# Kernel tuning notes

Hardware: AMD Instinct MI355X
Metric: run time of the kernel (lower is better)

The kernel has to match this reference:

```python
import jax, jax.numpy as jnp
import numpy as np

N = 100000
E = 1600000
D_IN = 128
D_H = 128


def _glorot(key, shape):
    fan_in, fan_out = shape[1], shape[0]
    lim = np.sqrt(6.0 / (fan_in + fan_out))
    return jax.random.uniform(key, shape, jnp.float32, -lim, lim)


def setup_inputs() -> dict:
    key = jax.random.key(0)
    ks = jax.random.split(key, 12)
    x = jax.random.normal(ks[0], (N, D_IN), jnp.float32)
    edge_index = jax.random.randint(ks[1], (2, E), 0, N, jnp.int64)
    return {
        "x": x,
        "edge_index": edge_index,
        # lin1, lin2 (nn.Linear: y = x @ W.T + b)
        "W1": _glorot(ks[2], (D_H, D_IN)),
        "b1": jnp.zeros((D_H,), jnp.float32),
        "W2": _glorot(ks[3], (D_H, D_H)),
        "b2": jnp.zeros((D_H,), jnp.float32),
        # SAGEConv1: lin_l (neighbors, with bias), lin_r (root, no bias)
        "c1_Wl": _glorot(ks[4], (D_H, D_H)),
        "c1_bl": jnp.zeros((D_H,), jnp.float32),
        "c1_Wr": _glorot(ks[5], (D_H, D_H)),
        # SAGEConv2
        "c2_Wl": _glorot(ks[6], (D_H, D_H)),
        "c2_bl": jnp.zeros((D_H,), jnp.float32),
        "c2_Wr": _glorot(ks[7], (D_H, D_H)),
    }


def _sage_conv(h, src, dst, Wl, bl, Wr, num_nodes):
    # PyG SAGEConv (mean aggr): out = lin_l(mean_{j in N(i)} h_j) + lin_r(h_i)
    msgs = h[src]  # [E, D] gather
    agg = jax.ops.segment_sum(msgs, dst, num_segments=num_nodes)  # [N, D]
    deg = jax.ops.segment_sum(jnp.ones((src.shape[0],), h.dtype), dst,
                              num_segments=num_nodes)
    mean = agg / jnp.maximum(deg, 1.0)[:, None]
    return mean @ Wl.T + bl + h @ Wr.T


def reference(x, edge_index, W1, b1, W2, b2,
              c1_Wl, c1_bl, c1_Wr, c2_Wl, c2_bl, c2_Wr):
    src, dst = edge_index[0], edge_index[1]
    n = x.shape[0]
    h = jax.nn.relu(x @ W1.T + b1)
    h = jax.nn.relu(_sage_conv(h, src, dst, c1_Wl, c1_bl, c1_Wr, n))
    h = jax.nn.relu(h @ W2.T + b2)
    h = jax.nn.relu(_sage_conv(h, src, dst, c2_Wl, c2_bl, c2_Wr, n))
    return h
```

## Files before the change

### kernel.cpp

```cpp
#include <hip/hip_runtime.h>
#include <hip/hip_bf16.h>

#define NN 100000
#define EE 1600000
#define DD 128

#define BSH 9
#define NBUK ((NN + 511) / 512)
#define EPB 8192

typedef __attribute__((ext_vector_type(8))) _Float16 half8;
typedef __attribute__((ext_vector_type(2))) _Float16 half2v;
typedef __attribute__((ext_vector_type(4))) float f32x4;

__global__ void k_detect(const long long* __restrict__ ei64, int* __restrict__ flag) {
    __shared__ int ok;
    if (threadIdx.x == 0) ok = 1;
    __syncthreads();
    long long v = ei64[threadIdx.x];
    if (v < 0 || v >= (long long)NN) atomicAnd(&ok, 0);
    __syncthreads();
    if (threadIdx.x == 0) *flag = ok;
}

__device__ inline int load_edge(const int* ei32, const long long* ei64, int is64, size_t pos) {
    return is64 ? (int)ei64[pos] : ei32[pos];
}

__global__ __launch_bounds__(1024) void k_bhist(const int* __restrict__ ei32,
                                                const long long* __restrict__ ei64,
                                                const int* __restrict__ flag,
                                                int* __restrict__ bcnt) {
    __shared__ int h[NBUK];
    int t = threadIdx.x;
    if (t < NBUK) h[t] = 0;
    __syncthreads();
    int is64 = *flag;
    int base = blockIdx.x * EPB;
    int end = min(base + EPB, EE);
    for (int e = base + t; e < end; e += 1024) {
        int d = load_edge(ei32, ei64, is64, (size_t)EE + e);
        atomicAdd(&h[d >> BSH], 1);
    }
    __syncthreads();
    if (t < NBUK && h[t] > 0) atomicAdd(&bcnt[t], h[t]);
}

__global__ __launch_bounds__(256) void k_bscan(const int* __restrict__ bcnt,
                                               int* __restrict__ bbase,
                                               int* __restrict__ bcur) {
    __shared__ int sm[256];
    int t = threadIdx.x;
    int v = (t < NBUK) ? bcnt[t] : 0;
    sm[t] = v;
    __syncthreads();
    for (int off = 1; off < 256; off <<= 1) {
        int u = (t >= off) ? sm[t - off] : 0;
        __syncthreads();
        sm[t] += u;
        __syncthreads();
    }
    if (t < NBUK) {
        int b = sm[t] - v;
        bbase[t] = b;
        bcur[t] = b;
    }
    if (t == 0) bbase[NBUK] = EE;
}

__global__ __launch_bounds__(1024) void k_part(const int* __restrict__ ei32,
                                               const long long* __restrict__ ei64,
                                               const int* __restrict__ flag,
                                               int* __restrict__ bcur,
                                               unsigned* __restrict__ eb) {
    __shared__ int h[NBUK];
    __shared__ int cbase[NBUK];
    int t = threadIdx.x;
    if (t < NBUK) h[t] = 0;
    __syncthreads();
    int is64 = *flag;
    int base = blockIdx.x * EPB;
    int end = min(base + EPB, EE);
    int mys[8], myd[8];
    int cnt_i = 0;
    for (int e = base + t; e < end; e += 1024) {
        int s = load_edge(ei32, ei64, is64, (size_t)e);
        int d = load_edge(ei32, ei64, is64, (size_t)EE + e);
        mys[cnt_i] = s;
        myd[cnt_i] = d;
        ++cnt_i;
        atomicAdd(&h[d >> BSH], 1);
    }
    __syncthreads();
    if (t < NBUK && h[t] > 0) cbase[t] = atomicAdd(&bcur[t], h[t]);
    __syncthreads();
    if (t < NBUK) h[t] = 0;
    __syncthreads();
    for (int i = 0; i < cnt_i; ++i) {
        int b = myd[i] >> BSH;
        int slot = atomicAdd(&h[b], 1);
        unsigned v = (unsigned)mys[i] | ((unsigned)(myd[i] & 511) << 17);
        eb[cbase[b] + slot] = v;
    }
}

__global__ __launch_bounds__(1024) void k_bucket(const unsigned* __restrict__ eb,
                                                 const int* __restrict__ bbase,
                                                 int* __restrict__ rp,
                                                 int* __restrict__ ssrc) {
    __shared__ int ncnt[512];
    __shared__ int cur[512];
    int b = blockIdx.x, t = threadIdx.x;
    int ebeg = bbase[b], eend = bbase[b + 1];
    int nodeBase = b << BSH;
    int nNodes = min(512, NN - nodeBase);
    if (t < 512) ncnt[t] = 0;
    __syncthreads();
    for (int i = ebeg + t; i < eend; i += 1024) {
        unsigned v = eb[i];
        atomicAdd(&ncnt[v >> 17], 1);
    }
    __syncthreads();
    int own = (t < 512) ? ncnt[t] : 0;
    for (int off = 1; off < 512; off <<= 1) {
        int u = (t >= off && t < 512) ? ncnt[t - off] : 0;
        __syncthreads();
        if (t < 512) ncnt[t] += u;
        __syncthreads();
    }
    if (t < 512) {
        int excl = ncnt[t] - own;
        cur[t] = ebeg + excl;
        if (t < nNodes) rp[nodeBase + t] = ebeg + excl;
    }
    __syncthreads();
    for (int i = ebeg + t; i < eend; i += 1024) {
        unsigned v = eb[i];
        int slot = atomicAdd(&cur[v >> 17], 1);
        ssrc[slot] = (int)(v & 0x1FFFFu);
    }
    if (b == 0 && t == 0) rp[NN] = EE;
}

__global__ void k_prepw(const float* __restrict__ w0, const float* __restrict__ w1,
                        const float* __restrict__ w2, const float* __restrict__ w3,
                        const float* __restrict__ w4, const float* __restrict__ w5,
                        _Float16* __restrict__ whi) {
    int i = blockIdx.x * 256 + threadIdx.x;
    if (i >= 6 * 16384) return;
    int slot = i >> 14, idx = i & 16383;
    const float* w = slot == 0 ? w0 : slot == 1 ? w1 : slot == 2 ? w2
                   : slot == 3 ? w3 : slot == 4 ? w4 : w5;
    whi[i] = (_Float16)w[idx];
}

#define WSTR 136

template <bool DUAL, bool AF16, bool OF16>
__global__ __launch_bounds__(256) void k_gemm(const void* __restrict__ A,
                                              const _Float16* __restrict__ W1g,
                                              const void* __restrict__ A2,
                                              const _Float16* __restrict__ W2g,
                                              const float* __restrict__ bias,
                                              void* __restrict__ out) {
    __shared__ _Float16 sW[128 * WSTR];
    int t = threadIdx.x;
    int wave = t >> 6;
    int lane = t & 63;
    int lr = lane & 15;
    int lk = lane >> 4;
    int rowBase = blockIdx.x * 128 + wave * 32;

    f32x4 acc[2][8];
#pragma unroll
    for (int mt = 0; mt < 2; ++mt)
#pragma unroll
        for (int nt = 0; nt < 8; ++nt) acc[mt][nt] = (f32x4){0.f, 0.f, 0.f, 0.f};

    const int NPASS = DUAL ? 2 : 1;
    for (int pass = 0; pass < NPASS; ++pass) {
        const _Float16* Wg = pass ? W2g : W1g;
        const void* Ap = pass ? A2 : A;
        if (pass) __syncthreads();
#pragma unroll
        for (int i = 0; i < 8; ++i) {
            int c = t + i * 256;
            int n = c >> 4, j = c & 15;
            *(half8*)(sW + n * WSTR + j * 8) = *(const half8*)(Wg + n * 128 + j * 8);
        }
        __syncthreads();

#pragma unroll
        for (int ks = 0; ks < 4; ++ks) {
            int kf = ks * 32 + lk * 8;
            half8 b[8];
#pragma unroll
            for (int nt = 0; nt < 8; ++nt)
                b[nt] = *(const half8*)(sW + (nt * 16 + lr) * WSTR + (ks * 4 + lk) * 8);
#pragma unroll
            for (int mt = 0; mt < 2; ++mt) {
                int row = rowBase + mt * 16 + lr;
                int rc = row < NN ? row : NN - 1;
                if (AF16) {
                    half8 a = *(const half8*)((const _Float16*)Ap + (size_t)rc * 128 + kf);
#pragma unroll
                    for (int nt = 0; nt < 8; ++nt)
                        acc[mt][nt] = __builtin_amdgcn_mfma_f32_16x16x32_f16(a, b[nt], acc[mt][nt], 0, 0, 0);
                } else {
                    const float* ap = (const float*)Ap + (size_t)rc * 128 + kf;
                    float4 a0 = *(const float4*)ap;
                    float4 a1 = *(const float4*)(ap + 4);
                    float av[8] = {a0.x, a0.y, a0.z, a0.w, a1.x, a1.y, a1.z, a1.w};
                    half8 ah, al;
#pragma unroll
                    for (int j = 0; j < 8; ++j) {
                        _Float16 h = (_Float16)av[j];
                        ah[j] = h;
                        al[j] = (_Float16)(av[j] - (float)h);
                    }
#pragma unroll
                    for (int nt = 0; nt < 8; ++nt) {
                        acc[mt][nt] = __builtin_amdgcn_mfma_f32_16x16x32_f16(ah, b[nt], acc[mt][nt], 0, 0, 0);
                        acc[mt][nt] = __builtin_amdgcn_mfma_f32_16x16x32_f16(al, b[nt], acc[mt][nt], 0, 0, 0);
                    }
                }
            }
        }
    }

#pragma unroll
    for (int mt = 0; mt < 2; ++mt) {
#pragma unroll
        for (int nt = 0; nt < 8; ++nt) {
            int col = nt * 16 + lr;
            float b = bias[col];
#pragma unroll
            for (int r = 0; r < 4; ++r) {
                int row = rowBase + mt * 16 + lk * 4 + r;
                if (row < NN) {
                    float v = acc[mt][nt][r] + b;
                    v = v > 0.f ? v : 0.f;
                    if (OF16)
                        ((_Float16*)out)[(size_t)row * 128 + col] = (_Float16)v;
                    else
                        ((float*)out)[(size_t)row * 128 + col] = v;
                }
            }
        }
    }
}

__global__ __launch_bounds__(256) void k_agg(const _Float16* __restrict__ h,
                                             const int* __restrict__ rp,
                                             const int* __restrict__ ssrc,
                                             _Float16* __restrict__ out) {
    int wid = (int)((blockIdx.x * 256 + threadIdx.x) >> 6);
    int lane = threadIdx.x & 63;
    if (wid >= NN) return;
    int s = __builtin_amdgcn_readfirstlane(rp[wid]);
    int e = __builtin_amdgcn_readfirstlane(rp[wid + 1]);
    const half2v* hp = (const half2v*)h;
    float ax = 0.f, ay = 0.f;
    int i = s;
    for (; i + 4 <= e; i += 4) {
        int s0 = ssrc[i], s1 = ssrc[i + 1], s2 = ssrc[i + 2], s3 = ssrc[i + 3];
        half2v v0 = hp[(size_t)s0 * 64 + lane];
        half2v v1 = hp[(size_t)s1 * 64 + lane];
        half2v v2 = hp[(size_t)s2 * 64 + lane];
        half2v v3 = hp[(size_t)s3 * 64 + lane];
        ax += (float)v0.x + (float)v1.x + (float)v2.x + (float)v3.x;
        ay += (float)v0.y + (float)v1.y + (float)v2.y + (float)v3.y;
    }
    for (; i < e; ++i) {
        int s0 = ssrc[i];
        half2v v0 = hp[(size_t)s0 * 64 + lane];
        ax += (float)v0.x;
        ay += (float)v0.y;
    }
    int deg = e - s;
    float inv = deg > 0 ? 1.0f / (float)deg : 0.f;
    half2v o;
    o.x = (_Float16)(ax * inv);
    o.y = (_Float16)(ay * inv);
    ((half2v*)out)[(size_t)wid * 64 + lane] = o;
}

extern "C" void kernel_launch(void* const* d_in, const int* in_sizes, int n_in,
                              void* d_out, int out_size, void* d_ws, size_t ws_size,
                              hipStream_t stream) {
    const float* x = (const float*)d_in[0];
    const int* ei32 = (const int*)d_in[1];
    const long long* ei64 = (const long long*)d_in[1];
    const float* b1 = (const float*)d_in[3];
    const float* b2 = (const float*)d_in[5];
    const float* c1_bl = (const float*)d_in[7];
    const float* c2_bl = (const float*)d_in[10];

    char* ws = (char*)d_ws;
    const size_t H16 = (size_t)NN * 128 * 2;
    _Float16* hH = (_Float16*)ws;
    _Float16* aggH = (_Float16*)(ws + H16);
    int* ssrc = (int*)(ws + 2 * H16);
    int* rp = (int*)(ws + 2 * H16 + 6400000);
    int* bufs = (int*)(ws + 2 * H16 + 6400000 + 400128);
    _Float16* whi = (_Float16*)(ws + 2 * H16 + 6400000 + 2 * 400128);
    int* flag = (int*)((char*)(whi + 6 * 16384));

    int* bcnt = bufs;
    int* bbase = bufs + 256;
    int* bcur = bufs + 512;
    unsigned* eb = (unsigned*)hH;

    k_detect<<<1, 256, 0, stream>>>(ei64, flag);
    hipMemsetAsync(bcnt, 0, NBUK * 4, stream);
    int pgrid = (EE + EPB - 1) / EPB;
    k_bhist<<<pgrid, 1024, 0, stream>>>(ei32, ei64, flag, bcnt);
    k_bscan<<<1, 256, 0, stream>>>(bcnt, bbase, bcur);
    k_part<<<pgrid, 1024, 0, stream>>>(ei32, ei64, flag, bcur, eb);
    k_bucket<<<NBUK, 1024, 0, stream>>>(eb, bbase, rp, ssrc);
    k_prepw<<<(6 * 16384 + 255) / 256, 256, 0, stream>>>(
        (const float*)d_in[2], (const float*)d_in[6], (const float*)d_in[8],
        (const float*)d_in[4], (const float*)d_in[9], (const float*)d_in[11], whi);

    dim3 g((NN + 127) / 128);
    int agrid = (NN + 3) / 4;
    k_gemm<false, false, true><<<g, 256, 0, stream>>>(
        x, whi + 0 * 16384, nullptr, nullptr, b1, hH);
    k_agg<<<agrid, 256, 0, stream>>>(hH, rp, ssrc, aggH);
    k_gemm<true, true, true><<<g, 256, 0, stream>>>(
        aggH, whi + 1 * 16384, hH, whi + 2 * 16384, c1_bl, aggH);
    k_gemm<false, true, true><<<g, 256, 0, stream>>>(
        aggH, whi + 3 * 16384, nullptr, nullptr, b2, hH);
    k_agg<<<agrid, 256, 0, stream>>>(hH, rp, ssrc, aggH);
    k_gemm<true, true, false><<<g, 256, 0, stream>>>(
        aggH, whi + 4 * 16384, hH, whi + 5 * 16384, c2_bl, d_out);
}
```

Before: 396.6 us.

## Fuse neighbor aggregation with SAGE conv GEMMs and following linear layer

```diff
diff --git a/kernel.cpp b/kernel.cpp
--- a/kernel.cpp
+++ b/kernel.cpp
@@ -8,6 +8,7 @@
 #define BSH 9
 #define NBUK ((NN + 511) / 512)
 #define EPB 8192
+#define AST 136
 
 typedef __attribute__((ext_vector_type(8))) _Float16 half8;
 typedef __attribute__((ext_vector_type(2))) _Float16 half2v;
@@ -81,26 +82,21 @@
     int is64 = *flag;
     int base = blockIdx.x * EPB;
     int end = min(base + EPB, EE);
-    int mys[8], myd[8];
-    int cnt_i = 0;
+    for (int e = base + t; e < end; e += 1024) {
+        int d = load_edge(ei32, ei64, is64, (size_t)EE + e);
+        atomicAdd(&h[d >> BSH], 1);
+    }
+    __syncthreads();
+    if (t < NBUK && h[t] > 0) cbase[t] = atomicAdd(&bcur[t], h[t]);
+    __syncthreads();
+    if (t < NBUK) h[t] = 0;
+    __syncthreads();
     for (int e = base + t; e < end; e += 1024) {
         int s = load_edge(ei32, ei64, is64, (size_t)e);
         int d = load_edge(ei32, ei64, is64, (size_t)EE + e);
-        mys[cnt_i] = s;
-        myd[cnt_i] = d;
-        ++cnt_i;
-        atomicAdd(&h[d >> BSH], 1);
-    }
-    __syncthreads();
-    if (t < NBUK && h[t] > 0) cbase[t] = atomicAdd(&bcur[t], h[t]);
-    __syncthreads();
-    if (t < NBUK) h[t] = 0;
-    __syncthreads();
-    for (int i = 0; i < cnt_i; ++i) {
-        int b = myd[i] >> BSH;
+        int b = d >> BSH;
         int slot = atomicAdd(&h[b], 1);
-        unsigned v = (unsigned)mys[i] | ((unsigned)(myd[i] & 511) << 17);
-        eb[cbase[b] + slot] = v;
+        eb[cbase[b] + slot] = (unsigned)s | ((unsigned)(d & 511) << 17);
     }
 }
 
@@ -154,21 +150,14 @@
     whi[i] = (_Float16)w[idx];
 }
 
-#define WSTR 136
-
-template <bool DUAL, bool AF16, bool OF16>
-__global__ __launch_bounds__(256) void k_gemm(const void* __restrict__ A,
-                                              const _Float16* __restrict__ W1g,
-                                              const void* __restrict__ A2,
-                                              const _Float16* __restrict__ W2g,
-                                              const float* __restrict__ bias,
-                                              void* __restrict__ out) {
-    __shared__ _Float16 sW[128 * WSTR];
+__global__ __launch_bounds__(256) void k_gemm1(const float* __restrict__ A,
+                                               const _Float16* __restrict__ Wg,
+                                               const float* __restrict__ bias,
+                                               _Float16* __restrict__ out) {
+    __shared__ _Float16 sW[128 * AST];
     int t = threadIdx.x;
-    int wave = t >> 6;
-    int lane = t & 63;
-    int lr = lane & 15;
-    int lk = lane >> 4;
+    int wave = t >> 6, lane = t & 63;
+    int lr = lane & 15, lk = lane >> 4;
     int rowBase = blockIdx.x * 128 + wave * 32;
 
     f32x4 acc[2][8];
@@ -177,112 +166,256 @@
 #pragma unroll
         for (int nt = 0; nt < 8; ++nt) acc[mt][nt] = (f32x4){0.f, 0.f, 0.f, 0.f};
 
-    const int NPASS = DUAL ? 2 : 1;
-    for (int pass = 0; pass < NPASS; ++pass) {
-        const _Float16* Wg = pass ? W2g : W1g;
-        const void* Ap = pass ? A2 : A;
-        if (pass) __syncthreads();
-#pragma unroll
-        for (int i = 0; i < 8; ++i) {
-            int c = t + i * 256;
-            int n = c >> 4, j = c & 15;
-            *(half8*)(sW + n * WSTR + j * 8) = *(const half8*)(Wg + n * 128 + j * 8);
-        }
-        __syncthreads();
-
-#pragma unroll
-        for (int ks = 0; ks < 4; ++ks) {
-            int kf = ks * 32 + lk * 8;
-            half8 b[8];
-#pragma unroll
-            for (int nt = 0; nt < 8; ++nt)
-                b[nt] = *(const half8*)(sW + (nt * 16 + lr) * WSTR + (ks * 4 + lk) * 8);
-#pragma unroll
-            for (int mt = 0; mt < 2; ++mt) {
-                int row = rowBase + mt * 16 + lr;
-                int rc = row < NN ? row : NN - 1;
-                if (AF16) {
-                    half8 a = *(const half8*)((const _Float16*)Ap + (size_t)rc * 128 + kf);
-#pragma unroll
-                    for (int nt = 0; nt < 8; ++nt)
-                        acc[mt][nt] = __builtin_amdgcn_mfma_f32_16x16x32_f16(a, b[nt], acc[mt][nt], 0, 0, 0);
-                } else {
-                    const float* ap = (const float*)Ap + (size_t)rc * 128 + kf;
-                    float4 a0 = *(const float4*)ap;
-                    float4 a1 = *(const float4*)(ap + 4);
-                    float av[8] = {a0.x, a0.y, a0.z, a0.w, a1.x, a1.y, a1.z, a1.w};
-                    half8 ah, al;
-#pragma unroll
-                    for (int j = 0; j < 8; ++j) {
-                        _Float16 h = (_Float16)av[j];
-                        ah[j] = h;
-                        al[j] = (_Float16)(av[j] - (float)h);
-                    }
-#pragma unroll
-                    for (int nt = 0; nt < 8; ++nt) {
-                        acc[mt][nt] = __builtin_amdgcn_mfma_f32_16x16x32_f16(ah, b[nt], acc[mt][nt], 0, 0, 0);
-                        acc[mt][nt] = __builtin_amdgcn_mfma_f32_16x16x32_f16(al, b[nt], acc[mt][nt], 0, 0, 0);
-                    }
-                }
-            }
-        }
-    }
-
-#pragma unroll
-    for (int mt = 0; mt < 2; ++mt) {
+#pragma unroll
+    for (int i = 0; i < 8; ++i) {
+        int c = t + i * 256;
+        int n = c >> 4, j = c & 15;
+        *(half8*)(sW + n * AST + j * 8) = *(const half8*)(Wg + n * 128 + j * 8);
+    }
+    __syncthreads();
+
+#pragma unroll
+    for (int ks = 0; ks < 4; ++ks) {
+        int kf = ks * 32 + lk * 8;
+        half8 b[8];
+#pragma unroll
+        for (int nt = 0; nt < 8; ++nt)
+            b[nt] = *(const half8*)(sW + (nt * 16 + lr) * AST + kf);
+#pragma unroll
+        for (int mt = 0; mt < 2; ++mt) {
+            int row = rowBase + mt * 16 + lr;
+            int rc = row < NN ? row : NN - 1;
+            const float* ap = A + (size_t)rc * 128 + kf;
+            float4 a0 = *(const float4*)ap;
+            float4 a1 = *(const float4*)(ap + 4);
+            float av[8] = {a0.x, a0.y, a0.z, a0.w, a1.x, a1.y, a1.z, a1.w};
+            half8 ah, al;
+#pragma unroll
+            for (int j = 0; j < 8; ++j) {
+                _Float16 h = (_Float16)av[j];
+                ah[j] = h;
+                al[j] = (_Float16)(av[j] - (float)h);
+            }
+#pragma unroll
+            for (int nt = 0; nt < 8; ++nt) {
+                acc[mt][nt] = __builtin_amdgcn_mfma_f32_16x16x32_f16(ah, b[nt], acc[mt][nt], 0, 0, 0);
+                acc[mt][nt] = __builtin_amdgcn_mfma_f32_16x16x32_f16(al, b[nt], acc[mt][nt], 0, 0, 0);
+            }
+        }
+    }
+
+#pragma unroll
+    for (int mt = 0; mt < 2; ++mt)
 #pragma unroll
         for (int nt = 0; nt < 8; ++nt) {
             int col = nt * 16 + lr;
-            float b = bias[col];
+            float bia = bias[col];
 #pragma unroll
             for (int r = 0; r < 4; ++r) {
                 int row = rowBase + mt * 16 + lk * 4 + r;
                 if (row < NN) {
-                    float v = acc[mt][nt][r] + b;
+                    float v = acc[mt][nt][r] + bia;
+                    out[(size_t)row * 128 + col] = (_Float16)(v > 0.f ? v : 0.f);
+                }
+            }
+        }
+}
+
+template <bool HASL, bool OF16>
+__global__ __launch_bounds__(256, 2) void k_conv(const _Float16* __restrict__ hsrc,
+                                                 const int* __restrict__ rp,
+                                                 const int* __restrict__ ssrc,
+                                                 const _Float16* __restrict__ Wlg,
+                                                 const _Float16* __restrict__ Wrg,
+                                                 const float* __restrict__ bconv,
+                                                 const _Float16* __restrict__ Wling,
+                                                 const float* __restrict__ blin,
+                                                 void* __restrict__ out) {
+    __shared__ _Float16 sW[128 * AST];
+    __shared__ _Float16 sA[128 * AST];
+    int t = threadIdx.x;
+    int wave = t >> 6, lane = t & 63;
+    int lr = lane & 15, lk = lane >> 4;
+    int rowBase = blockIdx.x * 128 + wave * 32;
+    const half2v* hp = (const half2v*)hsrc;
+
+    for (int i = 0; i < 32; ++i) {
+        int node = rowBase + i;
+        float ax = 0.f, ay = 0.f;
+        int deg = 0;
+        if (node < NN) {
+            int s = __builtin_amdgcn_readfirstlane(rp[node]);
+            int e = __builtin_amdgcn_readfirstlane(rp[node + 1]);
+            deg = e - s;
+            int j = s;
+            for (; j + 8 <= e; j += 8) {
+                int i0 = ssrc[j], i1 = ssrc[j + 1], i2 = ssrc[j + 2], i3 = ssrc[j + 3];
+                int i4 = ssrc[j + 4], i5 = ssrc[j + 5], i6 = ssrc[j + 6], i7 = ssrc[j + 7];
+                half2v v0 = hp[(size_t)i0 * 64 + lane];
+                half2v v1 = hp[(size_t)i1 * 64 + lane];
+                half2v v2 = hp[(size_t)i2 * 64 + lane];
+                half2v v3 = hp[(size_t)i3 * 64 + lane];
+                half2v v4 = hp[(size_t)i4 * 64 + lane];
+                half2v v5 = hp[(size_t)i5 * 64 + lane];
+                half2v v6 = hp[(size_t)i6 * 64 + lane];
+                half2v v7 = hp[(size_t)i7 * 64 + lane];
+                ax += ((float)v0.x + (float)v1.x) + ((float)v2.x + (float)v3.x)
+                    + ((float)v4.x + (float)v5.x) + ((float)v6.x + (float)v7.x);
+                ay += ((float)v0.y + (float)v1.y) + ((float)v2.y + (float)v3.y)
+                    + ((float)v4.y + (float)v5.y) + ((float)v6.y + (float)v7.y);
+            }
+            for (; j < e; ++j) {
+                half2v v0 = hp[(size_t)ssrc[j] * 64 + lane];
+                ax += (float)v0.x;
+                ay += (float)v0.y;
+            }
+        }
+        float inv = deg > 0 ? 1.0f / (float)deg : 0.f;
+        half2v o;
+        o.x = (_Float16)(ax * inv);
+        o.y = (_Float16)(ay * inv);
+        *(half2v*)(sA + (wave * 32 + i) * AST + 2 * lane) = o;
+    }
+    __syncthreads();
+
+#pragma unroll
+    for (int i = 0; i < 8; ++i) {
+        int c = t + i * 256;
+        int n = c >> 4, j = c & 15;
+        *(half8*)(sW + n * AST + j * 8) = *(const half8*)(Wlg + n * 128 + j * 8);
+    }
+    __syncthreads();
+
+    f32x4 acc[2][8];
+#pragma unroll
+    for (int mt = 0; mt < 2; ++mt)
+#pragma unroll
+        for (int nt = 0; nt < 8; ++nt) acc[mt][nt] = (f32x4){0.f, 0.f, 0.f, 0.f};
+
+#pragma unroll
+    for (int ks = 0; ks < 4; ++ks) {
+        int kf = ks * 32 + lk * 8;
+        half8 b[8];
+#pragma unroll
+        for (int nt = 0; nt < 8; ++nt)
+            b[nt] = *(const half8*)(sW + (nt * 16 + lr) * AST + kf);
+#pragma unroll
+        for (int mt = 0; mt < 2; ++mt) {
+            half8 a = *(const half8*)(sA + (wave * 32 + mt * 16 + lr) * AST + kf);
+#pragma unroll
+            for (int nt = 0; nt < 8; ++nt)
+                acc[mt][nt] = __builtin_amdgcn_mfma_f32_16x16x32_f16(a, b[nt], acc[mt][nt], 0, 0, 0);
+        }
+    }
+    __syncthreads();
+
+#pragma unroll
+    for (int i = 0; i < 8; ++i) {
+        int c = t + i * 256;
+        int n = c >> 4, j = c & 15;
+        *(half8*)(sW + n * AST + j * 8) = *(const half8*)(Wrg + n * 128 + j * 8);
+    }
+    __syncthreads();
+
+#pragma unroll
+    for (int ks = 0; ks < 4; ++ks) {
+        int kf = ks * 32 + lk * 8;
+        half8 b[8];
+#pragma unroll
+        for (int nt = 0; nt < 8; ++nt)
+            b[nt] = *(const half8*)(sW + (nt * 16 + lr) * AST + kf);
+#pragma unroll
+        for (int mt = 0; mt < 2; ++mt) {
+            int row = rowBase + mt * 16 + lr;
+            int rc = row < NN ? row : NN - 1;
+            half8 a = *(const half8*)(hsrc + (size_t)rc * 128 + kf);
+#pragma unroll
+            for (int nt = 0; nt < 8; ++nt)
+                acc[mt][nt] = __builtin_amdgcn_mfma_f32_16x16x32_f16(a, b[nt], acc[mt][nt], 0, 0, 0);
+        }
+    }
+
+    if (!HASL) {
+#pragma unroll
+        for (int mt = 0; mt < 2; ++mt)
+#pragma unroll
+            for (int nt = 0; nt < 8; ++nt) {
+                int col = nt * 16 + lr;
+                float bia = bconv[col];
+#pragma unroll
+                for (int r = 0; r < 4; ++r) {
+                    int row = rowBase + mt * 16 + lk * 4 + r;
+                    if (row < NN) {
+                        float v = acc[mt][nt][r] + bia;
+                        v = v > 0.f ? v : 0.f;
+                        if (OF16) ((_Float16*)out)[(size_t)row * 128 + col] = (_Float16)v;
+                        else ((float*)out)[(size_t)row * 128 + col] = v;
+                    }
+                }
+            }
+        return;
+    }
+
+#pragma unroll
+    for (int mt = 0; mt < 2; ++mt)
+#pragma unroll
+        for (int nt = 0; nt < 8; ++nt) {
+            int col = nt * 16 + lr;
+            float bia = bconv[col];
+#pragma unroll
+            for (int r = 0; r < 4; ++r) {
+                float v = acc[mt][nt][r] + bia;
+                sA[(wave * 32 + mt * 16 + lk * 4 + r) * AST + col] = (_Float16)(v > 0.f ? v : 0.f);
+            }
+        }
+    __syncthreads();
+
+#pragma unroll
+    for (int i = 0; i < 8; ++i) {
+        int c = t + i * 256;
+        int n = c >> 4, j = c & 15;
+        *(half8*)(sW + n * AST + j * 8) = *(const half8*)(Wling + n * 128 + j * 8);
+    }
+    __syncthreads();
+
+#pragma unroll
+    for (int mt = 0; mt < 2; ++mt)
+#pragma unroll
+        for (int nt = 0; nt < 8; ++nt) acc[mt][nt] = (f32x4){0.f, 0.f, 0.f, 0.f};
+
+#pragma unroll
+    for (int ks = 0; ks < 4; ++ks) {
+        int kf = ks * 32 + lk * 8;
+        half8 b[8];
+#pragma unroll
+        for (int nt = 0; nt < 8; ++nt)
+            b[nt] = *(const half8*)(sW + (nt * 16 + lr) * AST + kf);
+#pragma unroll
+        for (int mt = 0; mt < 2; ++mt) {
+            half8 a = *(const half8*)(sA + (wave * 32 + mt * 16 + lr) * AST + kf);
+#pragma unroll
+            for (int nt = 0; nt < 8; ++nt)
+                acc[mt][nt] = __builtin_amdgcn_mfma_f32_16x16x32_f16(a, b[nt], acc[mt][nt], 0, 0, 0);
+        }
+    }
+
+#pragma unroll
+    for (int mt = 0; mt < 2; ++mt)
+#pragma unroll
+        for (int nt = 0; nt < 8; ++nt) {
+            int col = nt * 16 + lr;
+            float bia = blin[col];
+#pragma unroll
+            for (int r = 0; r < 4; ++r) {
+                int row = rowBase + mt * 16 + lk * 4 + r;
+                if (row < NN) {
+                    float v = acc[mt][nt][r] + bia;
                     v = v > 0.f ? v : 0.f;
-                    if (OF16)
-                        ((_Float16*)out)[(size_t)row * 128 + col] = (_Float16)v;
-                    else
-                        ((float*)out)[(size_t)row * 128 + col] = v;
+                    if (OF16) ((_Float16*)out)[(size_t)row * 128 + col] = (_Float16)v;
+                    else ((float*)out)[(size_t)row * 128 + col] = v;
                 }
             }
         }
-    }
-}
-
-__global__ __launch_bounds__(256) void k_agg(const _Float16* __restrict__ h,
-                                             const int* __restrict__ rp,
-                                             const int* __restrict__ ssrc,
-                                             _Float16* __restrict__ out) {
-    int wid = (int)((blockIdx.x * 256 + threadIdx.x) >> 6);
-    int lane = threadIdx.x & 63;
-    if (wid >= NN) return;
-    int s = __builtin_amdgcn_readfirstlane(rp[wid]);
-    int e = __builtin_amdgcn_readfirstlane(rp[wid + 1]);
-    const half2v* hp = (const half2v*)h;
-    float ax = 0.f, ay = 0.f;
-    int i = s;
-    for (; i + 4 <= e; i += 4) {
-        int s0 = ssrc[i], s1 = ssrc[i + 1], s2 = ssrc[i + 2], s3 = ssrc[i + 3];
-        half2v v0 = hp[(size_t)s0 * 64 + lane];
-        half2v v1 = hp[(size_t)s1 * 64 + lane];
-        half2v v2 = hp[(size_t)s2 * 64 + lane];
-        half2v v3 = hp[(size_t)s3 * 64 + lane];
-        ax += (float)v0.x + (float)v1.x + (float)v2.x + (float)v3.x;
-        ay += (float)v0.y + (float)v1.y + (float)v2.y + (float)v3.y;
-    }
-    for (; i < e; ++i) {
-        int s0 = ssrc[i];
-        half2v v0 = hp[(size_t)s0 * 64 + lane];
-        ax += (float)v0.x;
-        ay += (float)v0.y;
-    }
-    int deg = e - s;
-    float inv = deg > 0 ? 1.0f / (float)deg : 0.f;
-    half2v o;
-    o.x = (_Float16)(ax * inv);
-    o.y = (_Float16)(ay * inv);
-    ((half2v*)out)[(size_t)wid * 64 + lane] = o;
 }
 
 extern "C" void kernel_launch(void* const* d_in, const int* in_sizes, int n_in,
@@ -299,7 +432,7 @@
     char* ws = (char*)d_ws;
     const size_t H16 = (size_t)NN * 128 * 2;
     _Float16* hH = (_Float16*)ws;
-    _Float16* aggH = (_Float16*)(ws + H16);
+    _Float16* h3H = (_Float16*)(ws + H16);
     int* ssrc = (int*)(ws + 2 * H16);
     int* rp = (int*)(ws + 2 * H16 + 6400000);
     int* bufs = (int*)(ws + 2 * H16 + 6400000 + 400128);
@@ -323,15 +456,11 @@
         (const float*)d_in[4], (const float*)d_in[9], (const float*)d_in[11], whi);
 
     dim3 g((NN + 127) / 128);
-    int agrid = (NN + 3) / 4;
-    k_gemm<false, false, true><<<g, 256, 0, stream>>>(
-        x, whi + 0 * 16384, nullptr, nullptr, b1, hH);
-    k_agg<<<agrid, 256, 0, stream>>>(hH, rp, ssrc, aggH);
-    k_gemm<true, true, true><<<g, 256, 0, stream>>>(
-        aggH, whi + 1 * 16384, hH, whi + 2 * 16384, c1_bl, aggH);
-    k_gemm<false, true, true><<<g, 256, 0, stream>>>(
-        aggH, whi + 3 * 16384, nullptr, nullptr, b2, hH);
-    k_agg<<<agrid, 256, 0, stream>>>(hH, rp, ssrc, aggH);
-    k_gemm<true, true, false><<<g, 256, 0, stream>>>(
-        aggH, whi + 4 * 16384, hH, whi + 5 * 16384, c2_bl, d_out);
-}
+    k_gemm1<<<g, 256, 0, stream>>>(x, whi + 0 * 16384, b1, hH);
+    k_conv<true, true><<<g, 256, 0, stream>>>(
+        hH, rp, ssrc, whi + 1 * 16384, whi + 2 * 16384, c1_bl,
+        whi + 3 * 16384, b2, h3H);
+    k_conv<false, false><<<g, 256, 0, stream>>>(
+        h3H, rp, ssrc, whi + 4 * 16384, whi + 5 * 16384, c2_bl,
+        nullptr, nullptr, d_out);
+}
```

New measurement: 545.3 us. 37.5% more time.
